# Kernel tuning notes

Hardware: AMD Instinct MI355X
Metric: run time of the kernel (lower is better)

## Reference

```python
import jax, jax.numpy as jnp
import numpy as np

COMMITMENT_COST = 0.25
NUM_EMBEDDINGS = 1024
EMBEDDING_DIM = 256


def setup_inputs() -> dict:
    key = jax.random.key(0)
    k1, k2 = jax.random.split(key)
    inputs = jax.random.normal(k1, (32, 32, 32, EMBEDDING_DIM), dtype=jnp.float32)
    # GlorotUniform-ish init for the [D, K] codebook
    limit = float(np.sqrt(6.0 / (EMBEDDING_DIM + NUM_EMBEDDINGS)))
    w = jax.random.uniform(k2, (EMBEDDING_DIM, NUM_EMBEDDINGS), dtype=jnp.float32,
                           minval=-limit, maxval=limit)
    return {"inputs": inputs, "w": w}


def reference(inputs, w):
    D, K = w.shape
    flat = inputs.reshape(-1, D)                                   # [N, D]
    distances = (jnp.sum(flat * flat, axis=1, keepdims=True)
                 - 2.0 * (flat @ w)
                 + jnp.sum(w * w, axis=0, keepdims=True))          # [N, K]
    enc_idx_flat = jnp.argmin(distances, axis=1)                   # [N]
    encodings = jax.nn.one_hot(enc_idx_flat, K, dtype=inputs.dtype)  # [N, K]
    encoding_indices = enc_idx_flat.reshape(inputs.shape[:-1])     # [B, H, W]
    quantized = jnp.take(w.T, encoding_indices, axis=0)            # [B, H, W, D]

    e_latent_loss = jnp.mean((jax.lax.stop_gradient(quantized) - inputs) ** 2)
    q_latent_loss = jnp.mean((quantized - jax.lax.stop_gradient(inputs)) ** 2)
    loss = q_latent_loss + COMMITMENT_COST * e_latent_loss

    quantized_skip = inputs + jax.lax.stop_gradient(quantized - inputs)

    avg_probs = jnp.mean(encodings, axis=0)                        # [K]
    perplexity = jnp.exp(-jnp.sum(avg_probs * jnp.log(avg_probs + 1e-10)))
    return (quantized_skip, loss, perplexity, encodings, encoding_indices)
```

## Files before the change

### kernel.cpp

```cpp
#include <hip/hip_runtime.h>
#include <cfloat>
#include <cmath>
#include <stdint.h>

#define NROWS 32768
#define DIM   256
#define KC    1024
#define MARGIN 0.125f

typedef short bf16x8 __attribute__((ext_vector_type(8)));
typedef float f32x4  __attribute__((ext_vector_type(4)));
typedef float f32x2  __attribute__((ext_vector_type(2)));

__device__ inline unsigned short f2bf(float f) {
    unsigned u = __float_as_uint(f);
    u = (u + 0x7fffu + ((u >> 16) & 1u)) >> 16;
    return (unsigned short)u;
}
__device__ inline float packsk(float s, int k) {
    return __int_as_float((__float_as_int(s) & ~1023) | k);
}

__global__ __launch_bounds__(256) void prep_w(const float* __restrict__ w,
                                              uint4* __restrict__ wph,
                                              float* __restrict__ wT) {
    const int t = blockIdx.x * 256 + threadIdx.x;
    const int l = t & 63;
    const int ks = (t >> 6) & 7;
    const int ctg = t >> 9;
    const int c = ctg * 16 + (l & 15);
    const int kbase = ks * 32 + ((l >> 4) << 3);
    union { unsigned short u[8]; uint4 v; } H;
#pragma unroll
    for (int j = 0; j < 8; ++j) {
        float v = w[(size_t)(kbase + j) * KC + c];
        H.u[j] = f2bf(v);
        wT[(size_t)c * DIM + kbase + j] = v;
    }
    wph[t] = H.v;
}

__global__ __launch_bounds__(256) void wnorm_kernel(const float* __restrict__ wT,
                                                    double* __restrict__ wnorm64,
                                                    float* __restrict__ wnormf) {
    const int k = blockIdx.x * 256 + threadIdx.x;
    const float* p = wT + (size_t)k * DIM;
    double acc = 0.0;
#pragma unroll 8
    for (int d = 0; d < DIM; ++d) acc += (double)p[d] * (double)p[d];
    wnorm64[k] = acc;
    wnormf[k] = (float)acc;
}

__global__ __launch_bounds__(256, 6) void vq_screen(
    const float* __restrict__ x,
    const char* __restrict__ wph,
    const float* __restrict__ wnormf,
    int* __restrict__ cand,
    float* __restrict__ out_enc)
{
    const int t = threadIdx.x;
    const int l = t & 63;
    const int wv = t >> 6;
    const int p = blockIdx.x & 3;
    const int rt = blockIdx.x >> 2;
    const int r0 = rt * 64 + wv * 16;
    const char* wp = wph + (size_t)p * 131072;

    bf16x8 ah[8];
    {
        const float* xb = x + (size_t)(r0 + (l & 15)) * DIM + ((l >> 4) << 3);
#pragma unroll
        for (int ks = 0; ks < 8; ++ks) {
            float4 p0 = *(const float4*)(xb + ks * 32);
            float4 p1 = *(const float4*)(xb + ks * 32 + 4);
            float f[8] = {p0.x, p0.y, p0.z, p0.w, p1.x, p1.y, p1.z, p1.w};
            union { unsigned short u[8]; bf16x8 v; } H;
#pragma unroll
            for (int j = 0; j < 8; ++j) H.u[j] = f2bf(f[j]);
            ah[ks] = H.v;
        }
    }

    float tv0[4], tv1[4], tv2[4];
#pragma unroll
    for (int r = 0; r < 4; ++r) { tv0[r] = tv1[r] = tv2[r] = FLT_MAX; }

    for (int g = 0; g < 16; ++g) {
        const char* bp = wp + (size_t)g * 8192 + l * 16;
        bf16x8 ba[4];
#pragma unroll
        for (int i = 0; i < 4; ++i) ba[i] = *(const bf16x8*)(bp + i * 1024);

        {
            const int zrow = r0 + g;
            f32x2* er2 = (f32x2*)(out_enc + (size_t)zrow * KC + p * 256);
            f32x2 z = {0.f, 0.f};
            __builtin_nontemporal_store(z, er2 + l);
            __builtin_nontemporal_store(z, er2 + 64 + l);
        }

        f32x4 acc = (f32x4){0.f, 0.f, 0.f, 0.f};
#pragma unroll
        for (int i = 0; i < 4; ++i)
            acc = __builtin_amdgcn_mfma_f32_16x16x32_bf16(ah[i], ba[i], acc, 0, 0, 0);
#pragma unroll
        for (int i = 0; i < 4; ++i) ba[i] = *(const bf16x8*)(bp + (4 + i) * 1024);
#pragma unroll
        for (int i = 0; i < 4; ++i)
            acc = __builtin_amdgcn_mfma_f32_16x16x32_bf16(ah[4 + i], ba[i], acc, 0, 0, 0);

        const int k = (p * 16 + g) * 16 + (l & 15);
        const float wn = wnormf[k];
#pragma unroll
        for (int r = 0; r < 4; ++r) {
            float sp = packsk(fmaf(-2.0f, acc[r], wn), k);
            if (sp < tv2[r]) {
                if (sp < tv1[r]) {
                    tv2[r] = tv1[r];
                    if (sp < tv0[r]) { tv1[r] = tv0[r]; tv0[r] = sp; }
                    else             { tv1[r] = sp; }
                } else { tv2[r] = sp; }
            }
        }
    }

    const int grpShift = (l >> 4) * 16;
    const unsigned laneMask = (1u << (l & 15)) - 1u;
#pragma unroll
    for (int r = 0; r < 4; ++r) {
        float v = tv0[r];
#pragma unroll
        for (int m = 1; m <= 8; m <<= 1) v = fminf(v, __shfl_xor(v, m));
        const float thr = v + MARGIN;
        const int row = r0 + ((l >> 4) << 2) + r;
        int* creg = cand + ((size_t)row * 4 + p) * 16;
        int base = 0;
#pragma unroll
        for (int j = 0; j < 3; ++j) {
            const float tvj = (j == 0) ? tv0[r] : (j == 1) ? tv1[r] : tv2[r];
            bool c = tvj <= thr;
            unsigned long long bal = __ballot(c);
            unsigned grp = (unsigned)(bal >> grpShift) & 0xFFFFu;
            int pos = base + __popc(grp & laneMask);
            if (c && pos < 7) {
                creg[1 + pos] = __float_as_int(tvj) & 1023;
                creg[8 + pos] = __float_as_int(tvj);
            }
            base += __popc(grp);
        }
        if ((l & 15) == 0) creg[0] = base < 7 ? base : 7;
    }
}

__global__ __launch_bounds__(256) void vq_final(
    const float* __restrict__ x, const float* __restrict__ wT,
    const double* __restrict__ wnorm64,
    const int* __restrict__ cand,
    float* __restrict__ out_q, float* __restrict__ out_idx, float* __restrict__ out_enc,
    int* __restrict__ counts, double* __restrict__ loss_sum)
{
    const int t = threadIdx.x;
    const int l = t & 63;
    const int wv = t >> 6;
    __shared__ double wsum[4];

    double ls0 = 0.0, ls1 = 0.0, ls2 = 0.0, ls3 = 0.0;
    const int stride = gridDim.x * 4;
    for (int row = blockIdx.x * 4 + wv; row < NROWS; row += stride) {
        const float4 xv = ((const float4*)(x + (size_t)row * DIM))[l];
        const int* c0 = cand + (size_t)row * 64;

        float m = FLT_MAX;
#pragma unroll
        for (int p4 = 0; p4 < 4; ++p4) {
            const int* cp = c0 + p4 * 16;
            const int n = cp[0];
            for (int c = 0; c < n; ++c) m = fminf(m, __int_as_float(cp[8 + c]));
        }
        const float thr = m + MARGIN;

        int bk = 0x7FFFFFFF, cnt = 0;
#pragma unroll
        for (int p4 = 0; p4 < 4; ++p4) {
            const int* cp = c0 + p4 * 16;
            const int n = cp[0];
            for (int c = 0; c < n; ++c)
                if (__int_as_float(cp[8 + c]) <= thr) { ++cnt; bk = cp[1 + c]; }
        }
        if (cnt > 1) {
            double best = 1e300; bk = 0x7FFFFFFF;
#pragma unroll
            for (int p4 = 0; p4 < 4; ++p4) {
                const int* cp = c0 + p4 * 16;
                const int n = cp[0];
                for (int c = 0; c < n; ++c) {
                    if (__int_as_float(cp[8 + c]) > thr) continue;
                    const int k2 = cp[1 + c];
                    const float4 w4 = ((const float4*)(wT + (size_t)k2 * DIM))[l];
                    double d = (double)xv.x * (double)w4.x;
                    d = fma((double)xv.y, (double)w4.y, d);
                    d = fma((double)xv.z, (double)w4.z, d);
                    d = fma((double)xv.w, (double)w4.w, d);
#pragma unroll
                    for (int mm = 32; mm > 0; mm >>= 1) d += __shfl_xor(d, mm);
                    const double s64 = wnorm64[k2] - 2.0 * d;
                    if (s64 < best || (s64 == best && k2 < bk)) { best = s64; bk = k2; }
                }
            }
        }
        const int k = __builtin_amdgcn_readfirstlane(bk);

        const float4 qv = ((const float4*)(wT + (size_t)k * DIM))[l];
        f32x4 o = {xv.x + (qv.x - xv.x), xv.y + (qv.y - xv.y),
                   xv.z + (qv.z - xv.z), xv.w + (qv.w - xv.w)};
        __builtin_nontemporal_store(o, (f32x4*)(out_q + (size_t)row * DIM) + l);
        double dx = (double)qv.x - (double)xv.x; ls0 = fma(dx, dx, ls0);
        dx = (double)qv.y - (double)xv.y; ls1 = fma(dx, dx, ls1);
        dx = (double)qv.z - (double)xv.z; ls2 = fma(dx, dx, ls2);
        dx = (double)qv.w - (double)xv.w; ls3 = fma(dx, dx, ls3);
        if (l == 0) {
            out_enc[(size_t)row * KC + k] = 1.0f;
            out_idx[row] = (float)k;
            atomicAdd(&counts[k], 1);
        }
    }
    double lsum = (ls0 + ls1) + (ls2 + ls3);
#pragma unroll
    for (int off = 32; off > 0; off >>= 1) lsum += __shfl_down(lsum, off);
    if (l == 0) wsum[wv] = lsum;
    __syncthreads();
    if (t == 0) atomicAdd(loss_sum, wsum[0] + wsum[1] + wsum[2] + wsum[3]);
}

__global__ __launch_bounds__(1024) void final_kernel(const int* __restrict__ counts,
                                                     const double* __restrict__ loss_sum,
                                                     float* __restrict__ out_loss,
                                                     float* __restrict__ out_ppl) {
    const int t = threadIdx.x;
    double p = (double)counts[t] * (1.0 / 32768.0);
    double term = -p * log(p + 1e-10);
#pragma unroll
    for (int off = 32; off > 0; off >>= 1) term += __shfl_down(term, off);
    __shared__ double ws[16];
    if ((t & 63) == 0) ws[t >> 6] = term;
    __syncthreads();
    if (t == 0) {
        double s = 0.0;
        for (int i = 0; i < 16; ++i) s += ws[i];
        *out_ppl = (float)exp(s);
        *out_loss = (float)(1.25 * loss_sum[0] * (1.0 / 8388608.0));
    }
}

extern "C" void kernel_launch(void* const* d_in, const int* in_sizes, int n_in,
                              void* d_out, int out_size, void* d_ws, size_t ws_size,
                              hipStream_t stream) {
    const float* x = (const float*)d_in[0];
    const float* w = (const float*)d_in[1];

    float* out = (float*)d_out;
    float* out_q    = out;
    float* out_loss = out + 8388608;
    float* out_ppl  = out + 8388609;
    float* out_enc  = out + 8388610;
    float* out_idx  = out + 8388610 + 33554432;

    char* wsb = (char*)d_ws;
    double* loss_sum = (double*)(wsb + 0);
    int*    counts   = (int*)(wsb + 64);
    double* wnorm64  = (double*)(wsb + 4160);
    float*  wnormf   = (float*)(wsb + 12352);
    float*  wT       = (float*)(wsb + 16448);
    uint4*  wph      = (uint4*)(wsb + 1065024);
    int*    cand     = (int*)(wsb + 1589312);

    (void)hipMemsetAsync(d_ws, 0, 4160, stream);

    prep_w<<<128, 256, 0, stream>>>(w, wph, wT);
    wnorm_kernel<<<4, 256, 0, stream>>>(wT, wnorm64, wnormf);
    vq_screen<<<2048, 256, 0, stream>>>(x, (const char*)wph, wnormf, cand, out_enc);
    vq_final<<<2048, 256, 0, stream>>>(x, wT, wnorm64, cand,
                                       out_q, out_idx, out_enc, counts, loss_sum);
    final_kernel<<<1, 1024, 0, stream>>>(counts, loss_sum, out_loss, out_ppl);
}
```

Measured before the change: 149.5 us.

## Split codebook into halves per block and parallelize codebook norm computation

```diff
diff --git a/kernel.cpp b/kernel.cpp
--- a/kernel.cpp
+++ b/kernel.cpp
@@ -43,16 +43,23 @@
 __global__ __launch_bounds__(256) void wnorm_kernel(const float* __restrict__ wT,
                                                     double* __restrict__ wnorm64,
                                                     float* __restrict__ wnormf) {
-    const int k = blockIdx.x * 256 + threadIdx.x;
-    const float* p = wT + (size_t)k * DIM;
+    const int t = threadIdx.x;
+    const int k = (blockIdx.x * 256 + t) >> 2;
+    const int q = t & 3;
+    const float4* p = (const float4*)(wT + (size_t)k * DIM) + q * 16;
     double acc = 0.0;
-#pragma unroll 8
-    for (int d = 0; d < DIM; ++d) acc += (double)p[d] * (double)p[d];
-    wnorm64[k] = acc;
-    wnormf[k] = (float)acc;
-}
-
-__global__ __launch_bounds__(256, 6) void vq_screen(
+#pragma unroll
+    for (int i = 0; i < 16; ++i) {
+        float4 v = p[i];
+        acc += (double)v.x * v.x + (double)v.y * v.y
+             + (double)v.z * v.z + (double)v.w * v.w;
+    }
+    acc += __shfl_xor(acc, 1);
+    acc += __shfl_xor(acc, 2);
+    if (q == 0) { wnorm64[k] = acc; wnormf[k] = (float)acc; }
+}
+
+__global__ __launch_bounds__(128, 6) void vq_screen(
     const float* __restrict__ x,
     const char* __restrict__ wph,
     const float* __restrict__ wnormf,
@@ -62,10 +69,10 @@
     const int t = threadIdx.x;
     const int l = t & 63;
     const int wv = t >> 6;
-    const int p = blockIdx.x & 3;
-    const int rt = blockIdx.x >> 2;
-    const int r0 = rt * 64 + wv * 16;
-    const char* wp = wph + (size_t)p * 131072;
+    const int p = blockIdx.x & 1;
+    const int rt = blockIdx.x >> 1;
+    const int r0 = rt * 32 + wv * 16;
+    const char* wp = wph + (size_t)p * 262144;
 
     bf16x8 ah[8];
     {
@@ -86,18 +93,19 @@
 #pragma unroll
     for (int r = 0; r < 4; ++r) { tv0[r] = tv1[r] = tv2[r] = FLT_MAX; }
 
-    for (int g = 0; g < 16; ++g) {
+    for (int g = 0; g < 32; ++g) {
         const char* bp = wp + (size_t)g * 8192 + l * 16;
         bf16x8 ba[4];
 #pragma unroll
         for (int i = 0; i < 4; ++i) ba[i] = *(const bf16x8*)(bp + i * 1024);
 
-        {
+        if (g < 16) {
             const int zrow = r0 + g;
-            f32x2* er2 = (f32x2*)(out_enc + (size_t)zrow * KC + p * 256);
+            f32x2* er2 = (f32x2*)(out_enc + (size_t)zrow * KC + p * 512);
             f32x2 z = {0.f, 0.f};
-            __builtin_nontemporal_store(z, er2 + l);
-            __builtin_nontemporal_store(z, er2 + 64 + l);
+#pragma unroll
+            for (int i = 0; i < 4; ++i)
+                __builtin_nontemporal_store(z, er2 + i * 64 + l);
         }
 
         f32x4 acc = (f32x4){0.f, 0.f, 0.f, 0.f};
@@ -110,7 +118,7 @@
         for (int i = 0; i < 4; ++i)
             acc = __builtin_amdgcn_mfma_f32_16x16x32_bf16(ah[4 + i], ba[i], acc, 0, 0, 0);
 
-        const int k = (p * 16 + g) * 16 + (l & 15);
+        const int k = (p * 32 + g) * 16 + (l & 15);
         const float wn = wnormf[k];
 #pragma unroll
         for (int r = 0; r < 4; ++r) {
@@ -134,7 +142,7 @@
         for (int m = 1; m <= 8; m <<= 1) v = fminf(v, __shfl_xor(v, m));
         const float thr = v + MARGIN;
         const int row = r0 + ((l >> 4) << 2) + r;
-        int* creg = cand + ((size_t)row * 4 + p) * 16;
+        int* creg = cand + ((size_t)row * 2 + p) * 16;
         int base = 0;
 #pragma unroll
         for (int j = 0; j < 3; ++j) {
@@ -169,12 +177,12 @@
     const int stride = gridDim.x * 4;
     for (int row = blockIdx.x * 4 + wv; row < NROWS; row += stride) {
         const float4 xv = ((const float4*)(x + (size_t)row * DIM))[l];
-        const int* c0 = cand + (size_t)row * 64;
+        const int* c0 = cand + (size_t)row * 32;
 
         float m = FLT_MAX;
 #pragma unroll
-        for (int p4 = 0; p4 < 4; ++p4) {
-            const int* cp = c0 + p4 * 16;
+        for (int p2 = 0; p2 < 2; ++p2) {
+            const int* cp = c0 + p2 * 16;
             const int n = cp[0];
             for (int c = 0; c < n; ++c) m = fminf(m, __int_as_float(cp[8 + c]));
         }
@@ -182,8 +190,8 @@
 
         int bk = 0x7FFFFFFF, cnt = 0;
 #pragma unroll
-        for (int p4 = 0; p4 < 4; ++p4) {
-            const int* cp = c0 + p4 * 16;
+        for (int p2 = 0; p2 < 2; ++p2) {
+            const int* cp = c0 + p2 * 16;
             const int n = cp[0];
             for (int c = 0; c < n; ++c)
                 if (__int_as_float(cp[8 + c]) <= thr) { ++cnt; bk = cp[1 + c]; }
@@ -191,8 +199,8 @@
         if (cnt > 1) {
             double best = 1e300; bk = 0x7FFFFFFF;
 #pragma unroll
-            for (int p4 = 0; p4 < 4; ++p4) {
-                const int* cp = c0 + p4 * 16;
+            for (int p2 = 0; p2 < 2; ++p2) {
+                const int* cp = c0 + p2 * 16;
                 const int n = cp[0];
                 for (int c = 0; c < n; ++c) {
                     if (__int_as_float(cp[8 + c]) > thr) continue;
@@ -278,8 +286,8 @@
     (void)hipMemsetAsync(d_ws, 0, 4160, stream);
 
     prep_w<<<128, 256, 0, stream>>>(w, wph, wT);
-    wnorm_kernel<<<4, 256, 0, stream>>>(wT, wnorm64, wnormf);
-    vq_screen<<<2048, 256, 0, stream>>>(x, (const char*)wph, wnormf, cand, out_enc);
+    wnorm_kernel<<<16, 256, 0, stream>>>(wT, wnorm64, wnormf);
+    vq_screen<<<2048, 128, 0, stream>>>(x, (const char*)wph, wnormf, cand, out_enc);
     vq_final<<<2048, 256, 0, stream>>>(x, wT, wnorm64, cand,
                                        out_q, out_idx, out_enc, counts, loss_sum);
     final_kernel<<<1, 1024, 0, stream>>>(counts, loss_sum, out_loss, out_ppl);
```

New measurement: 136.3 us. -8.8%, faster.

## Fuse codebook prep with norm kernel and share bf16 input fragments via LDS

Applied to the files above, without the earlier changes.

```diff
diff --git a/kernel.cpp b/kernel.cpp
--- a/kernel.cpp
+++ b/kernel.cpp
@@ -21,71 +21,84 @@
     return __int_as_float((__float_as_int(s) & ~1023) | k);
 }
 
-__global__ __launch_bounds__(256) void prep_w(const float* __restrict__ w,
-                                              uint4* __restrict__ wph,
-                                              float* __restrict__ wT) {
-    const int t = blockIdx.x * 256 + threadIdx.x;
-    const int l = t & 63;
-    const int ks = (t >> 6) & 7;
-    const int ctg = t >> 9;
+__global__ __launch_bounds__(512) void prep_wnorm(const float* __restrict__ w,
+                                                  uint4* __restrict__ wph,
+                                                  float* __restrict__ wT,
+                                                  double* __restrict__ wnorm64,
+                                                  float* __restrict__ wnormf) {
+    const int tl = threadIdx.x;
+    const int ctg = blockIdx.x;
+    const int t = ctg * 512 + tl;
+    const int l = tl & 63;
+    const int ks = (tl >> 6) & 7;
     const int c = ctg * 16 + (l & 15);
     const int kbase = ks * 32 + ((l >> 4) << 3);
     union { unsigned short u[8]; uint4 v; } H;
+    double s = 0.0;
 #pragma unroll
     for (int j = 0; j < 8; ++j) {
         float v = w[(size_t)(kbase + j) * KC + c];
         H.u[j] = f2bf(v);
         wT[(size_t)c * DIM + kbase + j] = v;
+        s = fma((double)v, (double)v, s);
     }
     wph[t] = H.v;
-}
-
-__global__ __launch_bounds__(256) void wnorm_kernel(const float* __restrict__ wT,
-                                                    double* __restrict__ wnorm64,
-                                                    float* __restrict__ wnormf) {
-    const int k = blockIdx.x * 256 + threadIdx.x;
-    const float* p = wT + (size_t)k * DIM;
-    double acc = 0.0;
-#pragma unroll 8
-    for (int d = 0; d < DIM; ++d) acc += (double)p[d] * (double)p[d];
-    wnorm64[k] = acc;
-    wnormf[k] = (float)acc;
-}
-
-__global__ __launch_bounds__(256, 6) void vq_screen(
+    s += __shfl_xor(s, 16);
+    s += __shfl_xor(s, 32);
+    __shared__ double part[8][16];
+    if (l < 16) part[ks][l] = s;
+    __syncthreads();
+    if (tl < 16) {
+        double tot = 0.0;
+#pragma unroll
+        for (int i = 0; i < 8; ++i) tot += part[i][tl];
+        wnorm64[ctg * 16 + tl] = tot;
+        wnormf[ctg * 16 + tl] = (float)tot;
+    }
+}
+
+__global__ __launch_bounds__(512, 6) void vq_screen(
     const float* __restrict__ x,
     const char* __restrict__ wph,
     const float* __restrict__ wnormf,
     int* __restrict__ cand,
     float* __restrict__ out_enc)
 {
+    __shared__ char fraglds[16384];
+
     const int t = threadIdx.x;
     const int l = t & 63;
-    const int wv = t >> 6;
-    const int p = blockIdx.x & 3;
-    const int rt = blockIdx.x >> 2;
-    const int r0 = rt * 64 + wv * 16;
-    const char* wp = wph + (size_t)p * 131072;
-
-    bf16x8 ah[8];
+    const int w = t >> 6;
+    const int rg = w >> 2;
+    const int p  = w & 3;
+    const int r0 = blockIdx.x * 32 + rg * 16;
+
     {
         const float* xb = x + (size_t)(r0 + (l & 15)) * DIM + ((l >> 4) << 3);
 #pragma unroll
-        for (int ks = 0; ks < 8; ++ks) {
+        for (int j = 0; j < 2; ++j) {
+            const int ks = 2 * p + j;
             float4 p0 = *(const float4*)(xb + ks * 32);
             float4 p1 = *(const float4*)(xb + ks * 32 + 4);
             float f[8] = {p0.x, p0.y, p0.z, p0.w, p1.x, p1.y, p1.z, p1.w};
-            union { unsigned short u[8]; bf16x8 v; } H;
-#pragma unroll
-            for (int j = 0; j < 8; ++j) H.u[j] = f2bf(f[j]);
-            ah[ks] = H.v;
-        }
-    }
+            union { unsigned short u[8]; uint4 v; } H;
+#pragma unroll
+            for (int i = 0; i < 8; ++i) H.u[i] = f2bf(f[i]);
+            *(uint4*)(fraglds + rg * 8192 + ks * 1024 + l * 16) = H.v;
+        }
+    }
+    __syncthreads();
+
+    bf16x8 ah[8];
+#pragma unroll
+    for (int ks = 0; ks < 8; ++ks)
+        ah[ks] = *(const bf16x8*)(fraglds + rg * 8192 + ks * 1024 + l * 16);
 
     float tv0[4], tv1[4], tv2[4];
 #pragma unroll
     for (int r = 0; r < 4; ++r) { tv0[r] = tv1[r] = tv2[r] = FLT_MAX; }
 
+    const char* wp = wph + (size_t)p * 131072;
     for (int g = 0; g < 16; ++g) {
         const char* bp = wp + (size_t)g * 8192 + l * 16;
         bf16x8 ba[4];
@@ -277,9 +290,8 @@
 
     (void)hipMemsetAsync(d_ws, 0, 4160, stream);
 
-    prep_w<<<128, 256, 0, stream>>>(w, wph, wT);
-    wnorm_kernel<<<4, 256, 0, stream>>>(wT, wnorm64, wnormf);
-    vq_screen<<<2048, 256, 0, stream>>>(x, (const char*)wph, wnormf, cand, out_enc);
+    prep_wnorm<<<64, 512, 0, stream>>>(w, wph, wT, wnorm64, wnormf);
+    vq_screen<<<1024, 512, 0, stream>>>(x, (const char*)wph, wnormf, cand, out_enc);
     vq_final<<<2048, 256, 0, stream>>>(x, wT, wnorm64, cand,
                                        out_q, out_idx, out_enc, counts, loss_sum);
     final_kernel<<<1, 1024, 0, stream>>>(counts, loss_sum, out_loss, out_ppl);
```

Result: faster. 131.3 us (-12.2%).
